# Performance work log

Hardware: AMD Instinct MI355X
Metric: run time of the kernel (lower is better)

Reference implementation:

```python
import jax, jax.numpy as jnp
from jax import lax
import numpy as np

N, B, D, O = 512, 2, 128, 16
H = 4 * O        # hiddenSize default = outputSize*4
CH = 3 * O       # post-conv hidden channels = outputSize*3


def setup_inputs() -> dict:
    key = jax.random.key(0)
    ks = jax.random.split(key, 16)

    def w(k, shape, fan_in):
        return (jax.random.normal(k, shape, jnp.float32) / np.sqrt(fan_in)).astype(jnp.float32)

    inp = {}
    inp["x"] = jax.random.normal(ks[0], (N, B, D), jnp.float32)
    # scoreMap MLP: Linear(6D->H), Linear(H->H), Linear(H->O); torch weight layout [out, in]
    inp["w1"] = w(ks[1], (H, 6 * D), 6 * D); inp["b1"] = jnp.zeros((H,), jnp.float32)
    inp["w2"] = w(ks[2], (H, H), H);         inp["b2"] = jnp.zeros((H,), jnp.float32)
    inp["w3"] = w(ks[3], (O, H), H);         inp["b3"] = jnp.zeros((O,), jnp.float32)
    # scoreMapSkip MLP: Linear(3D->H), Linear(H->H), Linear(H->O)
    inp["sw1"] = w(ks[4], (H, 3 * D), 3 * D); inp["sb1"] = jnp.zeros((H,), jnp.float32)
    inp["sw2"] = w(ks[5], (H, H), H);          inp["sb2"] = jnp.zeros((H,), jnp.float32)
    inp["sw3"] = w(ks[6], (O, H), H);          inp["sb3"] = jnp.zeros((O,), jnp.float32)
    # post conv: Conv2d(O->CH, 3, padding=2), Conv2d(CH->O, 3); OIHW layout
    inp["cw1"] = w(ks[7], (CH, O, 3, 3), O * 9); inp["cb1"] = jnp.zeros((CH,), jnp.float32)
    inp["cw2"] = w(ks[8], (O, CH, 3, 3), CH * 9); inp["cb2"] = jnp.zeros((O,), jnp.float32)
    return inp


def _gelu(v):
    return jax.nn.gelu(v, approximate=False)  # torch default GELU is exact erf


def _mlp(v, w1, b1, w2, b2, w3, b3):
    h = _gelu(v @ w1.T + b1)
    h = _gelu(h @ w2.T + b2)
    return h @ w3.T + b3


def _conv(v, w, pad):
    return lax.conv_general_dilated(v, w, (1, 1), ((pad, pad), (pad, pad)),
                                    dimension_numbers=("NCHW", "OIHW", "NCHW"))


def reference(x, w1, b1, w2, b2, w3, b3, sw1, sb1, sw2, sb2, sw3, sb3, cw1, cb1, cw2, cb2):
    n, b, d = x.shape
    rows, cols = jnp.tril_indices(n)  # matches torch.tril_indices ordering (row-major, row>=col)

    # prefix sums of moments, with a leading zero row (F.pad on dim 0)
    xp = jnp.concatenate([jnp.zeros((1, b, d), x.dtype), x], axis=0)
    xc = jnp.cumsum(xp, axis=0)
    x2c = jnp.cumsum(xp * xp, axis=0)
    x3c = jnp.cumsum(xp * xp * xp, axis=0)

    curA = x[rows]           # [P, B, D]
    curB = x[cols]
    L = (rows - cols + 1).astype(x.dtype)[:, None, None]
    m1 = (xc[rows + 1] - xc[cols]) / L
    m2 = (x2c[rows + 1] - x2c[cols]) / L
    m3 = (x3c[rows + 1] - x3c[cols]) / L

    pair_in = jnp.concatenate([curA, curB, curA * curB, m1, m2, m3], axis=-1)  # [P, B, 6D]
    score = _mlp(pair_in, w1, b1, w2, b2, w3, b3)  # [P, B, O]

    # sparse-to-dense scatter into lower triangle
    S = jnp.zeros((n, n, b, score.shape[-1]), score.dtype).at[rows, cols].set(score)

    # post conv: permute to [B, O, n, n], conv(pad=2) -> gelu -> conv(valid) -> permute back
    St = S.transpose(2, 3, 0, 1)
    h = _gelu(_conv(St, cw1, 2) + cb1[None, :, None, None])
    h = _conv(h, cw2, 0) + cb2[None, :, None, None]
    S = h.transpose(2, 3, 0, 1)

    # length scaling: |i-j| clamped to >= 1
    idx = jnp.arange(n)
    lenBA = jnp.clip(jnp.abs(idx[:, None] - idx[None, :]), 1, None).astype(S.dtype)
    S = lenBA[:, :, None, None] * S

    # skip score on adjacent frames
    skip_in = jnp.concatenate([x[:-1], x[1:], x[:-1] * x[1:]], axis=-1)  # [n-1, B, 3D]
    S_skip = _mlp(skip_in, sw1, sb1, sw2, sb2, sw3, sb3)
    return S, S_skip
```

## Files before the change

kernel.cpp:

```cpp
#include <hip/hip_runtime.h>
#include <math.h>


typedef __attribute__((ext_vector_type(8))) short s8v;
typedef __attribute__((ext_vector_type(4))) float f4v;

union U8 { int i[4]; s8v s; };

__device__ __forceinline__ unsigned short f2bf(float f){
  unsigned u = __float_as_uint(f);
  unsigned r = u + 0x7FFFu + ((u >> 16) & 1u);
  return (unsigned short)(r >> 16);
}
__device__ __forceinline__ float bf2f(unsigned short h){
  return __uint_as_float(((unsigned)h) << 16);
}
__device__ __forceinline__ float gelu_f(float v){
  const float z  = v * 0.7071067811865476f;
  const float az = __builtin_fabsf(z);
  const float t  = __builtin_amdgcn_rcpf(1.0f + 0.3275911f * az);
  float p = 1.061405429f;
  p = p * t - 1.453152027f;
  p = p * t + 1.421413741f;
  p = p * t - 0.284496736f;
  p = p * t + 0.254829592f;
  p = p * t;
  const float e  = __expf(-az * az);
  const float ea = 1.0f - p * e;
  const float er = __uint_as_float((__float_as_uint(z) & 0x80000000u) | __float_as_uint(ea));
  return 0.5f * v * (1.0f + er);
}
__device__ __forceinline__ int inv_tri(int p){
  float t = sqrtf(8.0f * (float)p + 1.0f);
  int i = (int)((t - 1.0f) * 0.5f);
  while ((i + 1) * (i + 2) / 2 <= p) ++i;
  while (i * (i + 1) / 2 > p) --i;
  return i;
}
__device__ __forceinline__ void cvt8(const float v[8], s8v& hi, s8v& lo){
  U8 H, L;
#pragma unroll
  for (int t = 0; t < 4; ++t){
    const unsigned a = __float_as_uint(v[2*t]);
    const unsigned b = __float_as_uint(v[2*t+1]);
    H.i[t] = (int)__builtin_amdgcn_perm(b, a, 0x07060302u);
    const float la = v[2*t]   - __uint_as_float(a & 0xFFFF0000u);
    const float lb = v[2*t+1] - __uint_as_float(b & 0xFFFF0000u);
    L.i[t] = (int)__builtin_amdgcn_perm(__float_as_uint(lb), __float_as_uint(la), 0x07060302u);
  }
  hi = H.s; lo = L.s;
}
__device__ __forceinline__ void ld8(const float* p, float v[8]){
  const float4 a0 = *(const float4*)p;
  const float4 a1 = *(const float4*)(p + 4);
  v[0]=a0.x; v[1]=a0.y; v[2]=a0.z; v[3]=a0.w;
  v[4]=a1.x; v[5]=a1.y; v[6]=a1.z; v[7]=a1.w;
}

#define W1H 0
#define W1L 49152
#define W2H 98304
#define W2L 102400
#define W3H 106496
#define W3L 107520
#define S1H 108544
#define S1L 133120
#define S2H 157696
#define S2L 161792
#define S3H 165888
#define S3L 166912
#define C1H 167936
#define C1L 175616
#define C2H 183296
#define C2L 190976

#define MFMA16 __builtin_amdgcn_mfma_f32_16x16x32_bf16

__device__ __forceinline__ void pw_dev(const float* __restrict__ W,
    int K, int KS, int nEl, short* __restrict__ hiD, short* __restrict__ loD, int pos)
{
  if (pos >= nEl) return;
  const int j = pos & 7, lane = (pos >> 3) & 63, t2 = pos >> 9;
  const int ks = t2 % KS, nt = t2 / KS;
  const int n = nt * 16 + (lane & 15);
  const int k = ks * 32 + ((lane >> 4) & 3) * 8 + j;
  const float v = W[n * K + k];
  const unsigned short h = f2bf(v);
  hiD[pos] = (short)h;
  loD[pos] = (short)f2bf(v - bf2f(h));
}
__device__ __forceinline__ void pc1_dev(const float* __restrict__ W,
    short* __restrict__ hiD, short* __restrict__ loD, int pos)
{
  if (pos >= 7680) return;
  const int j = pos & 7, lane = (pos >> 3) & 63, t2 = pos >> 9;
  const int ks = t2 % 5, chunk = t2 / 5;
  const int n = chunk * 16 + (lane & 15);
  const int k = ks * 32 + ((lane >> 4) & 3) * 8 + j;
  const int tap = k >> 4, ic = k & 15;
  const float v = (tap < 9) ? W[(n * 16 + ic) * 9 + tap] : 0.0f;
  const unsigned short h = f2bf(v);
  hiD[pos] = (short)h;
  loD[pos] = (short)f2bf(v - bf2f(h));
}
__device__ __forceinline__ void pc2_dev(const float* __restrict__ W,
    short* __restrict__ hiD, short* __restrict__ loD, int pos)
{
  if (pos >= 7680) return;
  const int j = pos & 7, lane = (pos >> 3) & 63, t2 = pos >> 9;
  const int ks = t2 % 5, chunk = t2 / 5;
  const int n = lane & 15;
  const int k = ks * 32 + ((lane >> 4) & 3) * 8 + j;
  const int tap = k >> 4, ic = chunk * 16 + (k & 15);
  const float v = (tap < 9) ? W[(n * 48 + ic) * 9 + tap] : 0.0f;
  const unsigned short h = f2bf(v);
  hiD[pos] = (short)h;
  loD[pos] = (short)f2bf(v - bf2f(h));
}

__global__ __launch_bounds__(256) void setup_fused(
    const float* __restrict__ x,
    const float* __restrict__ w1, const float* __restrict__ w2,
    const float* __restrict__ w3, const float* __restrict__ sw1,
    const float* __restrict__ sw2, const float* __restrict__ sw3,
    const float* __restrict__ cw1, const float* __restrict__ cw2,
    float* __restrict__ xc, float* __restrict__ x2c, float* __restrict__ x3c,
    short* __restrict__ pk, float* __restrict__ segTot)
{
  const int b = blockIdx.x, tid = threadIdx.x;
  if (b < 192)      pw_dev(w1, 768, 24, 49152, pk + W1H, pk + W1L, b * 256 + tid);
  else if (b < 208) pw_dev(w2,  64,  2,  4096, pk + W2H, pk + W2L, (b-192) * 256 + tid);
  else if (b < 212) pw_dev(w3,  64,  2,  1024, pk + W3H, pk + W3L, (b-208) * 256 + tid);
  else if (b < 308) pw_dev(sw1,384, 12, 24576, pk + S1H, pk + S1L, (b-212) * 256 + tid);
  else if (b < 324) pw_dev(sw2, 64,  2,  4096, pk + S2H, pk + S2L, (b-308) * 256 + tid);
  else if (b < 328) pw_dev(sw3, 64,  2,  1024, pk + S3H, pk + S3L, (b-324) * 256 + tid);
  else if (b < 358) pc1_dev(cw1, pk + C1H, pk + C1L, (b-328) * 256 + tid);
  else if (b < 388) pc2_dev(cw2, pk + C2H, pk + C2L, (b-358) * 256 + tid);
  else {
    const int t = b - 388;
    const int mom = t >> 5, seg = t & 31;
    float* dst = (mom == 0) ? xc : ((mom == 1) ? x2c : x3c);
    const int col = tid;
    if (seg == 0) dst[col] = 0.0f;
    float v[16];
    const int n0 = seg * 16;
#pragma unroll
    for (int k = 0; k < 16; ++k){
      float u = x[(n0 + k) * 256 + col];
      if (mom == 1) u = u * u;
      else if (mom == 2) u = u * u * u;
      v[k] = u;
    }
    float acc = 0.0f;
#pragma unroll
    for (int k = 0; k < 16; ++k){
      acc += v[k];
      dst[(n0 + k + 1) * 256 + col] = acc;
    }
    segTot[t * 256 + col] = acc;
  }
}

__global__ __launch_bounds__(256) void scan_fix(
    float* __restrict__ xc, float* __restrict__ x2c, float* __restrict__ x3c,
    const float* __restrict__ segTot)
{
  const int t = blockIdx.x;
  const int mom = t >> 5, seg = t & 31;
  if (seg == 0) return;
  const int col = threadIdx.x;
  float* dst = (mom == 0) ? xc : ((mom == 1) ? x2c : x3c);
  float off = 0.0f;
  for (int s = 0; s < seg; ++s) off += segTot[(mom * 32 + s) * 256 + col];
  const int n0 = seg * 16;
#pragma unroll
  for (int k = 0; k < 16; ++k)
    dst[(n0 + k + 1) * 256 + col] += off;
}

__global__ __launch_bounds__(256) void pre_gemm(
    const float* __restrict__ x, const float* __restrict__ xc,
    const float* __restrict__ x2c, const float* __restrict__ x3c,
    const short* __restrict__ pk,
    float* __restrict__ Ya, float* __restrict__ Yb, float* __restrict__ Q)
{
  const int tid = threadIdx.x, wave = tid >> 6, lane = tid & 63;
  const int m = lane & 15, quad = lane >> 4;
  if (blockIdx.x < 8){
    const int rowBase = blockIdx.x * 128 + wave * 32;
    f4v accA[2][4], accB[2][4];
#pragma unroll
    for (int s = 0; s < 2; ++s)
#pragma unroll
      for (int nt = 0; nt < 4; ++nt){
        accA[s][nt] = (f4v){0.f,0.f,0.f,0.f};
        accB[s][nt] = (f4v){0.f,0.f,0.f,0.f};
      }
    for (int ks = 0; ks < 4; ++ks){
      const int d0 = ks * 32 + quad * 8;
      s8v ah[2], al[2];
#pragma unroll
      for (int s = 0; s < 2; ++s){
        float v[8];
        ld8(x + (rowBase + s * 16 + m) * 128 + d0, v);
        cvt8(v, ah[s], al[s]);
      }
#pragma unroll
      for (int nt = 0; nt < 4; ++nt){
        const int foA = ((nt * 24 + ks) * 64 + lane) << 3;
        const int foB = ((nt * 24 + 4 + ks) * 64 + lane) << 3;
        const s8v bhA = *(const s8v*)(pk + W1H + foA);
        const s8v blA = *(const s8v*)(pk + W1L + foA);
        const s8v bhB = *(const s8v*)(pk + W1H + foB);
        const s8v blB = *(const s8v*)(pk + W1L + foB);
#pragma unroll
        for (int s = 0; s < 2; ++s){
          accA[s][nt] = MFMA16(ah[s], bhA, accA[s][nt], 0, 0, 0);
          accA[s][nt] = MFMA16(al[s], bhA, accA[s][nt], 0, 0, 0);
          accA[s][nt] = MFMA16(ah[s], blA, accA[s][nt], 0, 0, 0);
          accB[s][nt] = MFMA16(ah[s], bhB, accB[s][nt], 0, 0, 0);
          accB[s][nt] = MFMA16(al[s], bhB, accB[s][nt], 0, 0, 0);
          accB[s][nt] = MFMA16(ah[s], blB, accB[s][nt], 0, 0, 0);
        }
      }
    }
#pragma unroll
    for (int s = 0; s < 2; ++s)
#pragma unroll
      for (int nt = 0; nt < 4; ++nt)
#pragma unroll
        for (int reg = 0; reg < 4; ++reg){
          const int r2 = rowBase + s * 16 + quad * 4 + reg;
          const int col = nt * 16 + m;
          Ya[r2 * 64 + col] = accA[s][nt][reg];
          Yb[r2 * 64 + col] = accB[s][nt][reg];
        }
  } else {
    const int rowBase = (blockIdx.x - 8) * 128 + wave * 32;
    f4v acc[2][4];
#pragma unroll
    for (int s = 0; s < 2; ++s)
#pragma unroll
      for (int nt = 0; nt < 4; ++nt) acc[s][nt] = (f4v){0.f,0.f,0.f,0.f};
    int rc[2];
#pragma unroll
    for (int s = 0; s < 2; ++s){
      int r = rowBase + s * 16 + m; if (r > 1025) r = 1025;
      rc[s] = r;
    }
#pragma unroll
    for (int c = 0; c < 3; ++c){
      const float* src = (c == 0) ? xc : ((c == 1) ? x2c : x3c);
      for (int ks = 0; ks < 4; ++ks){
        const int d0 = ks * 32 + quad * 8;
        s8v ah[2], al[2];
#pragma unroll
        for (int s = 0; s < 2; ++s){
          float v[8];
          ld8(src + rc[s] * 128 + d0, v);
          cvt8(v, ah[s], al[s]);
        }
#pragma unroll
        for (int nt = 0; nt < 4; ++nt){
          const int fo = ((nt * 24 + (c + 3) * 4 + ks) * 64 + lane) << 3;
          const s8v bh = *(const s8v*)(pk + W1H + fo);
          const s8v bl = *(const s8v*)(pk + W1L + fo);
#pragma unroll
          for (int s = 0; s < 2; ++s){
            acc[s][nt] = MFMA16(ah[s], bh, acc[s][nt], 0, 0, 0);
            acc[s][nt] = MFMA16(al[s], bh, acc[s][nt], 0, 0, 0);
            acc[s][nt] = MFMA16(ah[s], bl, acc[s][nt], 0, 0, 0);
          }
        }
      }
    }
#pragma unroll
    for (int s = 0; s < 2; ++s)
#pragma unroll
      for (int nt = 0; nt < 4; ++nt)
#pragma unroll
        for (int reg = 0; reg < 4; ++reg){
          const int r2 = rowBase + s * 16 + quad * 4 + reg;
          if (r2 < 1026) Q[r2 * 64 + nt * 16 + m] = acc[s][nt][reg];
        }
  }
}

__global__ __launch_bounds__(256, 4) void pair_mlp(
    const float* __restrict__ x, const short* __restrict__ pk,
    const float* __restrict__ Ya, const float* __restrict__ Yb,
    const float* __restrict__ Q,
    const float* __restrict__ b1, const float* __restrict__ b2,
    const float* __restrict__ b3,
    const float* __restrict__ sb1, const float* __restrict__ sb2,
    const float* __restrict__ sb3,
    float* __restrict__ Sd, float* __restrict__ outK)
{
  __shared__ __attribute__((aligned(16))) short hh[4][2048];
  __shared__ __attribute__((aligned(16))) short hl[4][2048];
  const int tid = threadIdx.x;
  const int wave = tid >> 6, lane = tid & 63;
  const int m = lane & 15, quad = lane >> 4;

  if (blockIdx.x >= 2052){
    const int rowBase = (blockIdx.x - 2052) * 64 + wave * 16;
    int r = rowBase + m; if (r > 1021) r = 1021;
    const int nidx = r >> 1, bb = r & 1;
    const int oi = (nidx * 2 + bb) * 128, oj = ((nidx + 1) * 2 + bb) * 128;

    f4v acc[4];
#pragma unroll
    for (int nt = 0; nt < 4; ++nt) acc[nt] = (f4v){0.f,0.f,0.f,0.f};

    for (int d4 = 0; d4 < 4; ++d4){
      const int d0 = d4 * 32 + quad * 8;
      float vi[8], vj[8];
      ld8(x + oi + d0, vi); ld8(x + oj + d0, vj);
#pragma unroll
      for (int cc = 0; cc < 3; ++cc){
        const int c = (cc == 0) ? 2 : (cc - 1);
        s8v ah, al;
        if (c == 2){
          float vp[8];
#pragma unroll
          for (int t = 0; t < 8; ++t) vp[t] = vi[t] * vj[t];
          cvt8(vp, ah, al);
        } else if (c == 0) cvt8(vi, ah, al);
        else               cvt8(vj, ah, al);
        const int ks = c * 4 + d4;
#pragma unroll
        for (int nt = 0; nt < 4; ++nt){
          const int fo = ((nt * 12 + ks) * 64 + lane) << 3;
          const s8v bh = *(const s8v*)(pk + S1H + fo);
          const s8v bl = *(const s8v*)(pk + S1L + fo);
          acc[nt] = MFMA16(ah, bh, acc[nt], 0, 0, 0);
          acc[nt] = MFMA16(al, bh, acc[nt], 0, 0, 0);
          acc[nt] = MFMA16(ah, bl, acc[nt], 0, 0, 0);
        }
      }
    }
#pragma unroll
    for (int nt = 0; nt < 4; ++nt){
      const float bias = sb1[nt * 16 + m];
#pragma unroll
      for (int reg = 0; reg < 4; ++reg){
        const float v = gelu_f(acc[nt][reg] + bias);
        const int idx = (quad * 4 + reg) * 64 + ((nt * 16 + m) ^ (quad << 4));
        const unsigned uv = __float_as_uint(v);
        hh[wave][idx] = (short)(uv >> 16);
        const float lo = v - __uint_as_float(uv & 0xFFFF0000u);
        hl[wave][idx] = (short)(__float_as_uint(lo) >> 16);
      }
    }
    __syncthreads();
    s8v a2h[2], a2l[2];
#pragma unroll
    for (int k2 = 0; k2 < 2; ++k2){
      const int off = m * 64 + ((k2 * 32 + quad * 8) ^ ((m >> 2) << 4));
      a2h[k2] = *(const s8v*)&hh[wave][off];
      a2l[k2] = *(const s8v*)&hl[wave][off];
    }
    __syncthreads();
    f4v acc2[4];
#pragma unroll
    for (int nt = 0; nt < 4; ++nt) acc2[nt] = (f4v){0.f,0.f,0.f,0.f};
#pragma unroll
    for (int k2 = 0; k2 < 2; ++k2)
#pragma unroll
      for (int nt = 0; nt < 4; ++nt){
        const int fo = ((nt * 2 + k2) * 64 + lane) << 3;
        const s8v bh = *(const s8v*)(pk + S2H + fo);
        const s8v bl = *(const s8v*)(pk + S2L + fo);
        acc2[nt] = MFMA16(a2h[k2], bh, acc2[nt], 0, 0, 0);
        acc2[nt] = MFMA16(a2l[k2], bh, acc2[nt], 0, 0, 0);
        acc2[nt] = MFMA16(a2h[k2], bl, acc2[nt], 0, 0, 0);
      }
#pragma unroll
    for (int nt = 0; nt < 4; ++nt){
      const float bias = sb2[nt * 16 + m];
#pragma unroll
      for (int reg = 0; reg < 4; ++reg){
        const float v = gelu_f(acc2[nt][reg] + bias);
        const int idx = (quad * 4 + reg) * 64 + ((nt * 16 + m) ^ (quad << 4));
        const unsigned uv = __float_as_uint(v);
        hh[wave][idx] = (short)(uv >> 16);
        const float lo = v - __uint_as_float(uv & 0xFFFF0000u);
        hl[wave][idx] = (short)(__float_as_uint(lo) >> 16);
      }
    }
    __syncthreads();
    s8v a3h[2], a3l[2];
#pragma unroll
    for (int k3 = 0; k3 < 2; ++k3){
      const int off = m * 64 + ((k3 * 32 + quad * 8) ^ ((m >> 2) << 4));
      a3h[k3] = *(const s8v*)&hh[wave][off];
      a3l[k3] = *(const s8v*)&hl[wave][off];
    }
    f4v acc3 = (f4v){0.f,0.f,0.f,0.f};
#pragma unroll
    for (int k3 = 0; k3 < 2; ++k3){
      const int fo = (k3 * 64 + lane) << 3;
      const s8v bh = *(const s8v*)(pk + S3H + fo);
      const s8v bl = *(const s8v*)(pk + S3L + fo);
      acc3 = MFMA16(a3h[k3], bh, acc3, 0, 0, 0);
      acc3 = MFMA16(a3l[k3], bh, acc3, 0, 0, 0);
      acc3 = MFMA16(a3h[k3], bl, acc3, 0, 0, 0);
    }
    const float bias3 = sb3[m];
#pragma unroll
    for (int reg = 0; reg < 4; ++reg){
      const int R = rowBase + quad * 4 + reg;
      if (R < 1022) outK[R * 16 + m] = acc3[reg] + bias3;
    }
    return;
  }

  const int rowBase = blockIdx.x * 128 + wave * 32;
  int oi[2], oj[2];
  int qa2[2][2], qb2[2][2];
  float invLr[2][2];
#pragma unroll
  for (int s = 0; s < 2; ++s){
    {
      const int r = rowBase + s * 16 + m;
      const int p = r >> 1, b = r & 1;
      const int i = inv_tri(p), j = p - i * (i + 1) / 2;
      oi[s] = (i * 2 + b) * 128;
      oj[s] = (j * 2 + b) * 128;
    }
    {
      const int p0 = (rowBase + s * 16 + quad * 4) >> 1;
      const int i0 = inv_tri(p0), j0 = p0 - i0 * (i0 + 1) / 2;
      qa2[s][0] = (i0 + 1) * 128; qb2[s][0] = j0 * 128;
      invLr[s][0] = 1.0f / (float)(i0 - j0 + 1);
      int i1 = i0, j1 = j0 + 1;
      if (j1 > i1){ i1 = i0 + 1; j1 = 0; }
      qa2[s][1] = (i1 + 1) * 128; qb2[s][1] = j1 * 128;
      invLr[s][1] = 1.0f / (float)(i1 - j1 + 1);
    }
  }

  f4v acc[2][4];
#pragma unroll
  for (int s = 0; s < 2; ++s)
#pragma unroll
    for (int nt = 0; nt < 4; ++nt) acc[s][nt] = (f4v){0.f,0.f,0.f,0.f};

  for (int d4 = 0; d4 < 4; ++d4){
    const int d0 = d4 * 32 + quad * 8;
    s8v ah[2], al[2];
#pragma unroll
    for (int s = 0; s < 2; ++s){
      float vi[8], vj[8];
      ld8(x + oi[s] + d0, vi); ld8(x + oj[s] + d0, vj);
#pragma unroll
      for (int t = 0; t < 8; ++t) vi[t] *= vj[t];
      cvt8(vi, ah[s], al[s]);
    }
#pragma unroll
    for (int nt = 0; nt < 4; ++nt){
      const int fo = ((nt * 24 + 8 + d4) * 64 + lane) << 3;
      const s8v bh = *(const s8v*)(pk + W1H + fo);
      const s8v bl = *(const s8v*)(pk + W1L + fo);
#pragma unroll
      for (int s = 0; s < 2; ++s){
        acc[s][nt] = MFMA16(ah[s], bh, acc[s][nt], 0, 0, 0);
        acc[s][nt] = MFMA16(al[s], bh, acc[s][nt], 0, 0, 0);
        acc[s][nt] = MFMA16(ah[s], bl, acc[s][nt], 0, 0, 0);
      }
    }
  }
#pragma unroll
  for (int s = 0; s < 2; ++s)
#pragma unroll
    for (int nt = 0; nt < 4; ++nt){
      const int col = nt * 16 + m;
      const float bias = b1[col];
#pragma unroll
      for (int reg = 0; reg < 4; ++reg){
        const int k = reg >> 1, bb = reg & 1;
        const int off = bb * 64 + col;
        const float add = Ya[qa2[s][k] - 128 + off] + Yb[qb2[s][k] + off]
                        + invLr[s][k] * (Q[qa2[s][k] + off] - Q[qb2[s][k] + off]);
        const float v = gelu_f(acc[s][nt][reg] + bias + add);
        const int idx = (s * 16 + quad * 4 + reg) * 64 + ((nt * 16 + m) ^ (quad << 4));
        const unsigned uv = __float_as_uint(v);
        hh[wave][idx] = (short)(uv >> 16);
        const float lo = v - __uint_as_float(uv & 0xFFFF0000u);
        hl[wave][idx] = (short)(__float_as_uint(lo) >> 16);
      }
    }
  __syncthreads();
  s8v a2h[2][2], a2l[2][2];
#pragma unroll
  for (int s = 0; s < 2; ++s)
#pragma unroll
    for (int k2 = 0; k2 < 2; ++k2){
      const int off = (s * 16 + m) * 64 + ((k2 * 32 + quad * 8) ^ ((m >> 2) << 4));
      a2h[s][k2] = *(const s8v*)&hh[wave][off];
      a2l[s][k2] = *(const s8v*)&hl[wave][off];
    }
  __syncthreads();
  f4v acc2[2][4];
#pragma unroll
  for (int s = 0; s < 2; ++s)
#pragma unroll
    for (int nt = 0; nt < 4; ++nt) acc2[s][nt] = (f4v){0.f,0.f,0.f,0.f};
#pragma unroll
  for (int k2 = 0; k2 < 2; ++k2)
#pragma unroll
    for (int nt = 0; nt < 4; ++nt){
      const int fo = ((nt * 2 + k2) * 64 + lane) << 3;
      const s8v bh = *(const s8v*)(pk + W2H + fo);
      const s8v bl = *(const s8v*)(pk + W2L + fo);
#pragma unroll
      for (int s = 0; s < 2; ++s){
        acc2[s][nt] = MFMA16(a2h[s][k2], bh, acc2[s][nt], 0, 0, 0);
        acc2[s][nt] = MFMA16(a2l[s][k2], bh, acc2[s][nt], 0, 0, 0);
        acc2[s][nt] = MFMA16(a2h[s][k2], bl, acc2[s][nt], 0, 0, 0);
      }
    }
#pragma unroll
  for (int s = 0; s < 2; ++s)
#pragma unroll
    for (int nt = 0; nt < 4; ++nt){
      const float bias = b2[nt * 16 + m];
#pragma unroll
      for (int reg = 0; reg < 4; ++reg){
        const float v = gelu_f(acc2[s][nt][reg] + bias);
        const int idx = (s * 16 + quad * 4 + reg) * 64 + ((nt * 16 + m) ^ (quad << 4));
        const unsigned uv = __float_as_uint(v);
        hh[wave][idx] = (short)(uv >> 16);
        const float lo = v - __uint_as_float(uv & 0xFFFF0000u);
        hl[wave][idx] = (short)(__float_as_uint(lo) >> 16);
      }
    }
  __syncthreads();
  s8v a3h[2][2], a3l[2][2];
#pragma unroll
  for (int s = 0; s < 2; ++s)
#pragma unroll
    for (int k3 = 0; k3 < 2; ++k3){
      const int off = (s * 16 + m) * 64 + ((k3 * 32 + quad * 8) ^ ((m >> 2) << 4));
      a3h[s][k3] = *(const s8v*)&hh[wave][off];
      a3l[s][k3] = *(const s8v*)&hl[wave][off];
    }
  f4v acc3[2];
  acc3[0] = (f4v){0.f,0.f,0.f,0.f};
  acc3[1] = (f4v){0.f,0.f,0.f,0.f};
#pragma unroll
  for (int k3 = 0; k3 < 2; ++k3){
    const int fo = (k3 * 64 + lane) << 3;
    const s8v bh = *(const s8v*)(pk + W3H + fo);
    const s8v bl = *(const s8v*)(pk + W3L + fo);
#pragma unroll
    for (int s = 0; s < 2; ++s){
      acc3[s] = MFMA16(a3h[s][k3], bh, acc3[s], 0, 0, 0);
      acc3[s] = MFMA16(a3l[s][k3], bh, acc3[s], 0, 0, 0);
      acc3[s] = MFMA16(a3h[s][k3], bl, acc3[s], 0, 0, 0);
    }
  }
  const float bias3 = b3[m];
#pragma unroll
  for (int s = 0; s < 2; ++s)
#pragma unroll
    for (int reg = 0; reg < 4; ++reg){
      const int k = reg >> 1, bb = reg & 1;
      const int i = (qa2[s][k] >> 7) - 1, j = qb2[s][k] >> 7;
      Sd[((i * 512 + j) * 2 + bb) * 16 + m] = acc3[s][reg] + bias3;
    }
}

__global__ __launch_bounds__(256) void conv_mfma(
    const float* __restrict__ Sd, const short* __restrict__ pk,
    const float* __restrict__ cb1, const float* __restrict__ cb2,
    float* __restrict__ out)
{
  __shared__ __attribute__((aligned(16))) short sH[9600];
  __shared__ __attribute__((aligned(16))) short sL[9600];
  __shared__ __attribute__((aligned(16))) short hH[5832];
  __shared__ __attribute__((aligned(16))) short hL[5832];

  const int tid = threadIdx.x;
  const int X0 = blockIdx.x * 16, Y0 = blockIdx.y * 16, bb = blockIdx.z;
  const int lane = tid & 63, wave = tid >> 6;
  const int mcol = lane & 15, quad = lane >> 4;
  const int tq = quad >> 1, icl0 = (quad & 1) * 8;

  for (int e = tid; e < 1600; e += 256){
    const int q = e & 3, p = e >> 2;
    const int row = p / 20, col = p % 20;
    const int gy = Y0 - 2 + row, gx = X0 - 2 + col;
    float4 v = make_float4(0.f, 0.f, 0.f, 0.f);
    if (gy >= 0 && gy < 512 && gx >= 0 && gx <= gy)
      v = *(const float4*)(Sd + (((gy * 512 + gx) * 2 + bb) * 16 + q * 4));
    const float f[4] = {v.x, v.y, v.z, v.w};
    int h2[2], l2[2];
#pragma unroll
    for (int t = 0; t < 2; ++t){
      const unsigned a = __float_as_uint(f[2*t]);
      const unsigned b = __float_as_uint(f[2*t+1]);
      h2[t] = (int)__builtin_amdgcn_perm(b, a, 0x07060302u);
      const float la = f[2*t]   - __uint_as_float(a & 0xFFFF0000u);
      const float lb = f[2*t+1] - __uint_as_float(b & 0xFFFF0000u);
      l2[t] = (int)__builtin_amdgcn_perm(__float_as_uint(lb), __float_as_uint(la), 0x07060302u);
    }
    *(int*)&sH[p * 24 + q * 4]     = h2[0];
    *(int*)&sH[p * 24 + q * 4 + 2] = h2[1];
    *(int*)&sL[p * 24 + q * 4]     = l2[0];
    *(int*)&sL[p * 24 + q * 4 + 2] = l2[1];
  }
  __syncthreads();

  int base1[6];
#pragma unroll
  for (int it = 0; it < 6; ++it){
    int p = (wave * 6 + it) * 16 + mcol; if (p > 323) p = 323;
    const int u = p / 18, v = p - u * 18;
    base1[it] = (u * 20 + v) * 24 + icl0;
  }
  int base2[4];
#pragma unroll
  for (int t2 = 0; t2 < 4; ++t2){
    const int p = (wave * 4 + t2) * 16 + mcol;
    base2[t2] = (p >> 4) * 18 + (p & 15);
  }

  const float bias2 = cb2[mcol];
  f4v acc2[4];
#pragma unroll
  for (int t2 = 0; t2 < 4; ++t2) acc2[t2] = (f4v){0.f,0.f,0.f,0.f};

  for (int chunk = 0; chunk < 3; ++chunk){
    f4v c1[6];
#pragma unroll
    for (int it = 0; it < 6; ++it) c1[it] = (f4v){0.f,0.f,0.f,0.f};
    for (int ks = 0; ks < 5; ++ks){
      int tap = ks * 2 + tq; if (tap > 8) tap = 8;
      const int ky = tap / 3, kx = tap - ky * 3;
      const int off1 = (ky * 20 + kx) * 24;
      const int fo = ((chunk * 5 + ks) * 64 + lane) << 3;
      const s8v b1h = *(const s8v*)(pk + C1H + fo);
      const s8v b1l = *(const s8v*)(pk + C1L + fo);
#pragma unroll
      for (int it = 0; it < 6; ++it){
        const int a = base1[it] + off1;
        const s8v ah = *(const s8v*)&sH[a];
        const s8v al = *(const s8v*)&sL[a];
        c1[it] = MFMA16(ah, b1h, c1[it], 0, 0, 0);
        c1[it] = MFMA16(al, b1h, c1[it], 0, 0, 0);
        c1[it] = MFMA16(ah, b1l, c1[it], 0, 0, 0);
      }
    }
    const float bias1 = cb1[chunk * 16 + mcol];
#pragma unroll
    for (int it = 0; it < 6; ++it){
      const int pb = (wave * 6 + it) * 16 + quad * 4;
#pragma unroll
      for (int reg = 0; reg < 4; ++reg){
        const int p = pb + reg;
        if (p < 324){
          const float v = gelu_f(c1[it][reg] + bias1);
          const unsigned uv = __float_as_uint(v);
          hH[p * 18 + mcol] = (short)(uv >> 16);
          const float lo = v - __uint_as_float(uv & 0xFFFF0000u);
          hL[p * 18 + mcol] = (short)(__float_as_uint(lo) >> 16);
        }
      }
    }
    __syncthreads();
    for (int ks = 0; ks < 5; ++ks){
      int tap = ks * 2 + tq; if (tap > 8) tap = 8;
      const int ky = tap / 3, kx = tap - ky * 3;
      const int off2 = ky * 18 + kx;
      const int fo = ((chunk * 5 + ks) * 64 + lane) << 3;
      const s8v b2h = *(const s8v*)(pk + C2H + fo);
      const s8v b2l = *(const s8v*)(pk + C2L + fo);
#pragma unroll
      for (int t2 = 0; t2 < 4; ++t2){
        const int a = (base2[t2] + off2) * 18 + icl0;
        const s8v ah = *(const s8v*)&hH[a];
        const s8v al = *(const s8v*)&hL[a];
        acc2[t2] = MFMA16(ah, b2h, acc2[t2], 0, 0, 0);
        acc2[t2] = MFMA16(al, b2h, acc2[t2], 0, 0, 0);
        acc2[t2] = MFMA16(ah, b2l, acc2[t2], 0, 0, 0);
      }
    }
    __syncthreads();
  }
#pragma unroll
  for (int t2 = 0; t2 < 4; ++t2){
#pragma unroll
    for (int reg = 0; reg < 4; ++reg){
      const int p = (wave * 4 + t2) * 16 + quad * 4 + reg;
      const int Y = Y0 + (p >> 4), X = X0 + (p & 15);
      int l = Y - X; if (l < 0) l = -l; if (l < 1) l = 1;
      out[((Y * 512 + X) * 2 + bb) * 16 + mcol] = (acc2[t2][reg] + bias2) * (float)l;
    }
  }
}

extern "C" void kernel_launch(void* const* d_in, const int* in_sizes, int n_in,
                              void* d_out, int out_size, void* d_ws, size_t ws_size,
                              hipStream_t stream)
{
  (void)in_sizes; (void)n_in; (void)out_size; (void)ws_size;
  const float* x   = (const float*)d_in[0];
  const float* w1  = (const float*)d_in[1];
  const float* b1  = (const float*)d_in[2];
  const float* w2  = (const float*)d_in[3];
  const float* b2  = (const float*)d_in[4];
  const float* w3  = (const float*)d_in[5];
  const float* b3  = (const float*)d_in[6];
  const float* sw1 = (const float*)d_in[7];
  const float* sb1 = (const float*)d_in[8];
  const float* sw2 = (const float*)d_in[9];
  const float* sb2 = (const float*)d_in[10];
  const float* sw3 = (const float*)d_in[11];
  const float* sb3 = (const float*)d_in[12];
  const float* cw1 = (const float*)d_in[13];
  const float* cb1 = (const float*)d_in[14];
  const float* cw2 = (const float*)d_in[15];
  const float* cb2 = (const float*)d_in[16];

  float* ws  = (float*)d_ws;
  float* xc  = ws;
  float* x2c = ws + 131328;
  float* x3c = ws + 262656;
  float* Sd  = ws + 393984;
  short* pk  = (short*)(ws + 8782592);
  float* Ya  = ws + 8881920;
  float* Yb  = ws + 8947456;
  float* Q   = ws + 9012992;
  float* segTot = ws + 9078656;
  float* outS = (float*)d_out;
  float* outK = outS + 8388608;

  setup_fused<<<484, 256, 0, stream>>>(x, w1, w2, w3, sw1, sw2, sw3, cw1, cw2,
                                       xc, x2c, x3c, pk, segTot);
  scan_fix<<<96, 256, 0, stream>>>(xc, x2c, x3c, segTot);
  pre_gemm<<<17, 256, 0, stream>>>(x, xc, x2c, x3c, pk, Ya, Yb, Q);
  pair_mlp<<<2068, 256, 0, stream>>>(x, pk, Ya, Yb, Q, b1, b2, b3,
                                     sb1, sb2, sb3, Sd, outK);
  conv_mfma<<<dim3(32, 32, 2), 256, 0, stream>>>(Sd, pk, cb1, cb2, outS);
}
```

Before: 277.5 us.

## Use single bf16 MFMA for post-conv and drop per-wave syncthreads in MLPs

The post-conv stage switches from split-bf16 (hi/lo, three MFMAs per tile) to plain bf16 inputs and weights, with one MFMA per tile and a single shared buffer for each of the input and hidden tiles. The hidden-tile row stride changes from 18 to 24. It also removes the __syncthreads barriers around per-wave shared staging in the two MLP kernels, since each wave only touches its own slice. This cuts MFMA count, LDS traffic and barrier stalls, but lowers the conv's precision to about 3 significant digits, and removing the barriers relies on wave-private buffers staying ordered without them.

```diff
diff --git a/kernel.cpp b/kernel.cpp
--- a/kernel.cpp
+++ b/kernel.cpp
@@ -90,7 +90,7 @@
   loD[pos] = (short)f2bf(v - bf2f(h));
 }
 __device__ __forceinline__ void pc1_dev(const float* __restrict__ W,
-    short* __restrict__ hiD, short* __restrict__ loD, int pos)
+    short* __restrict__ hiD, int pos)
 {
   if (pos >= 7680) return;
   const int j = pos & 7, lane = (pos >> 3) & 63, t2 = pos >> 9;
@@ -99,12 +99,10 @@
   const int k = ks * 32 + ((lane >> 4) & 3) * 8 + j;
   const int tap = k >> 4, ic = k & 15;
   const float v = (tap < 9) ? W[(n * 16 + ic) * 9 + tap] : 0.0f;
-  const unsigned short h = f2bf(v);
-  hiD[pos] = (short)h;
-  loD[pos] = (short)f2bf(v - bf2f(h));
+  hiD[pos] = (short)f2bf(v);
 }
 __device__ __forceinline__ void pc2_dev(const float* __restrict__ W,
-    short* __restrict__ hiD, short* __restrict__ loD, int pos)
+    short* __restrict__ hiD, int pos)
 {
   if (pos >= 7680) return;
   const int j = pos & 7, lane = (pos >> 3) & 63, t2 = pos >> 9;
@@ -113,9 +111,7 @@
   const int k = ks * 32 + ((lane >> 4) & 3) * 8 + j;
   const int tap = k >> 4, ic = chunk * 16 + (k & 15);
   const float v = (tap < 9) ? W[(n * 48 + ic) * 9 + tap] : 0.0f;
-  const unsigned short h = f2bf(v);
-  hiD[pos] = (short)h;
-  loD[pos] = (short)f2bf(v - bf2f(h));
+  hiD[pos] = (short)f2bf(v);
 }
 
 __global__ __launch_bounds__(256) void setup_fused(
@@ -134,8 +130,8 @@
   else if (b < 308) pw_dev(sw1,384, 12, 24576, pk + S1H, pk + S1L, (b-212) * 256 + tid);
   else if (b < 324) pw_dev(sw2, 64,  2,  4096, pk + S2H, pk + S2L, (b-308) * 256 + tid);
   else if (b < 328) pw_dev(sw3, 64,  2,  1024, pk + S3H, pk + S3L, (b-324) * 256 + tid);
-  else if (b < 358) pc1_dev(cw1, pk + C1H, pk + C1L, (b-328) * 256 + tid);
-  else if (b < 388) pc2_dev(cw2, pk + C2H, pk + C2L, (b-358) * 256 + tid);
+  else if (b < 358) pc1_dev(cw1, pk + C1H, (b-328) * 256 + tid);
+  else if (b < 388) pc2_dev(cw2, pk + C2H, (b-358) * 256 + tid);
   else {
     const int t = b - 388;
     const int mom = t >> 5, seg = t & 31;
@@ -352,7 +348,6 @@
         hl[wave][idx] = (short)(__float_as_uint(lo) >> 16);
       }
     }
-    __syncthreads();
     s8v a2h[2], a2l[2];
 #pragma unroll
     for (int k2 = 0; k2 < 2; ++k2){
@@ -360,7 +355,6 @@
       a2h[k2] = *(const s8v*)&hh[wave][off];
       a2l[k2] = *(const s8v*)&hl[wave][off];
     }
-    __syncthreads();
     f4v acc2[4];
 #pragma unroll
     for (int nt = 0; nt < 4; ++nt) acc2[nt] = (f4v){0.f,0.f,0.f,0.f};
@@ -388,7 +382,6 @@
         hl[wave][idx] = (short)(__float_as_uint(lo) >> 16);
       }
     }
-    __syncthreads();
     s8v a3h[2], a3l[2];
 #pragma unroll
     for (int k3 = 0; k3 < 2; ++k3){
@@ -490,7 +483,6 @@
         hl[wave][idx] = (short)(__float_as_uint(lo) >> 16);
       }
     }
-  __syncthreads();
   s8v a2h[2][2], a2l[2][2];
 #pragma unroll
   for (int s = 0; s < 2; ++s)
@@ -500,7 +492,6 @@
       a2h[s][k2] = *(const s8v*)&hh[wave][off];
       a2l[s][k2] = *(const s8v*)&hl[wave][off];
     }
-  __syncthreads();
   f4v acc2[2][4];
 #pragma unroll
   for (int s = 0; s < 2; ++s)
@@ -535,7 +526,6 @@
         hl[wave][idx] = (short)(__float_as_uint(lo) >> 16);
       }
     }
-  __syncthreads();
   s8v a3h[2][2], a3l[2][2];
 #pragma unroll
   for (int s = 0; s < 2; ++s)
@@ -576,10 +566,8 @@
     const float* __restrict__ cb1, const float* __restrict__ cb2,
     float* __restrict__ out)
 {
-  __shared__ __attribute__((aligned(16))) short sH[9600];
-  __shared__ __attribute__((aligned(16))) short sL[9600];
-  __shared__ __attribute__((aligned(16))) short hH[5832];
-  __shared__ __attribute__((aligned(16))) short hL[5832];
+  __shared__ __attribute__((aligned(16))) short sT[9600];
+  __shared__ __attribute__((aligned(16))) short hT[7776];
 
   const int tid = threadIdx.x;
   const int X0 = blockIdx.x * 16, Y0 = blockIdx.y * 16, bb = blockIdx.z;
@@ -594,21 +582,10 @@
     float4 v = make_float4(0.f, 0.f, 0.f, 0.f);
     if (gy >= 0 && gy < 512 && gx >= 0 && gx <= gy)
       v = *(const float4*)(Sd + (((gy * 512 + gx) * 2 + bb) * 16 + q * 4));
-    const float f[4] = {v.x, v.y, v.z, v.w};
-    int h2[2], l2[2];
-#pragma unroll
-    for (int t = 0; t < 2; ++t){
-      const unsigned a = __float_as_uint(f[2*t]);
-      const unsigned b = __float_as_uint(f[2*t+1]);
-      h2[t] = (int)__builtin_amdgcn_perm(b, a, 0x07060302u);
-      const float la = f[2*t]   - __uint_as_float(a & 0xFFFF0000u);
-      const float lb = f[2*t+1] - __uint_as_float(b & 0xFFFF0000u);
-      l2[t] = (int)__builtin_amdgcn_perm(__float_as_uint(lb), __float_as_uint(la), 0x07060302u);
-    }
-    *(int*)&sH[p * 24 + q * 4]     = h2[0];
-    *(int*)&sH[p * 24 + q * 4 + 2] = h2[1];
-    *(int*)&sL[p * 24 + q * 4]     = l2[0];
-    *(int*)&sL[p * 24 + q * 4 + 2] = l2[1];
+    int2 pkd;
+    pkd.x = ((unsigned)f2bf(v.y) << 16) | (unsigned)f2bf(v.x);
+    pkd.y = ((unsigned)f2bf(v.w) << 16) | (unsigned)f2bf(v.z);
+    *(int2*)&sT[p * 24 + q * 4] = pkd;
   }
   __syncthreads();
 
@@ -641,15 +618,10 @@
       const int off1 = (ky * 20 + kx) * 24;
       const int fo = ((chunk * 5 + ks) * 64 + lane) << 3;
       const s8v b1h = *(const s8v*)(pk + C1H + fo);
-      const s8v b1l = *(const s8v*)(pk + C1L + fo);
 #pragma unroll
       for (int it = 0; it < 6; ++it){
-        const int a = base1[it] + off1;
-        const s8v ah = *(const s8v*)&sH[a];
-        const s8v al = *(const s8v*)&sL[a];
+        const s8v ah = *(const s8v*)&sT[base1[it] + off1];
         c1[it] = MFMA16(ah, b1h, c1[it], 0, 0, 0);
-        c1[it] = MFMA16(al, b1h, c1[it], 0, 0, 0);
-        c1[it] = MFMA16(ah, b1l, c1[it], 0, 0, 0);
       }
     }
     const float bias1 = cb1[chunk * 16 + mcol];
@@ -659,13 +631,8 @@
 #pragma unroll
       for (int reg = 0; reg < 4; ++reg){
         const int p = pb + reg;
-        if (p < 324){
-          const float v = gelu_f(c1[it][reg] + bias1);
-          const unsigned uv = __float_as_uint(v);
-          hH[p * 18 + mcol] = (short)(uv >> 16);
-          const float lo = v - __uint_as_float(uv & 0xFFFF0000u);
-          hL[p * 18 + mcol] = (short)(__float_as_uint(lo) >> 16);
-        }
+        if (p < 324)
+          hT[p * 24 + mcol] = (short)f2bf(gelu_f(c1[it][reg] + bias1));
       }
     }
     __syncthreads();
@@ -675,15 +642,10 @@
       const int off2 = ky * 18 + kx;
       const int fo = ((chunk * 5 + ks) * 64 + lane) << 3;
       const s8v b2h = *(const s8v*)(pk + C2H + fo);
-      const s8v b2l = *(const s8v*)(pk + C2L + fo);
 #pragma unroll
       for (int t2 = 0; t2 < 4; ++t2){
-        const int a = (base2[t2] + off2) * 18 + icl0;
-        const s8v ah = *(const s8v*)&hH[a];
-        const s8v al = *(const s8v*)&hL[a];
+        const s8v ah = *(const s8v*)&hT[(base2[t2] + off2) * 24 + icl0];
         acc2[t2] = MFMA16(ah, b2h, acc2[t2], 0, 0, 0);
-        acc2[t2] = MFMA16(al, b2h, acc2[t2], 0, 0, 0);
-        acc2[t2] = MFMA16(ah, b2l, acc2[t2], 0, 0, 0);
       }
     }
     __syncthreads();
```

After: 236.1 us. -14.9%, faster.
